# Kernel tuning notes

Measured on AMD Instinct MI355X. Metric: run time of the kernel, lower is better.

The kernel has to match this reference:

```python
import jax, jax.numpy as jnp
import numpy as np

S, D_IN, D_OUT = 4096, 1024, 1024

def setup_inputs() -> dict:
    key = jax.random.key(0)
    kx, kq, kk, kv = jax.random.split(key, 4)
    scale = 0.02
    return {
        "x": jax.random.normal(kx, (S, D_IN), dtype=jnp.float32),
        "W_query": jax.random.normal(kq, (D_IN, D_OUT), dtype=jnp.float32) * scale,
        "W_key": jax.random.normal(kk, (D_IN, D_OUT), dtype=jnp.float32) * scale,
        "W_value": jax.random.normal(kv, (D_IN, D_OUT), dtype=jnp.float32) * scale,
    }

def reference(x, W_query, W_key, W_value):
    # x: [S, d_in]; W_*: [d_in, d_out]
    queries = x @ W_query        # [S, d_out]
    keys = x @ W_key             # [S, d_out]
    values = x @ W_value         # [S, d_out]
    d_k = keys.shape[-1]
    attn_scores = queries @ keys.T            # [S, S]
    attn_weights = jax.nn.softmax(attn_scores / jnp.sqrt(jnp.float32(d_k)), axis=-1)
    context_vec = attn_weights @ values       # [S, d_out]
    return context_vec
```

## Files before the change

### kernel.cpp

```cpp
#include <hip/hip_runtime.h>
#include <hip/hip_bf16.h>

typedef _Float16 f16x8 __attribute__((ext_vector_type(8)));
typedef float f32x4 __attribute__((ext_vector_type(4)));
typedef unsigned short u16;
typedef u16 u16x8 __attribute__((ext_vector_type(8)));
typedef u16 u16x4 __attribute__((ext_vector_type(4)));

__device__ __forceinline__ u16 f2h_bits(float f) {
    _Float16 h = (_Float16)f;
    return __builtin_bit_cast(u16, h);
}
__device__ __forceinline__ float h2f(u16 b) {
    return (float)__builtin_bit_cast(_Float16, b);
}

template <int MODE>
__global__ __launch_bounds__(256, 4) void gemm_bt(
    const u16* __restrict__ A, int lda,
    const u16* __restrict__ B, int ldb,
    u16* __restrict__ C, int ldc,
    int Ksplit, float alpha, size_t c_z_stride,
    int bnW, int bmW, int numPanelX,
    float* __restrict__ rowsum, u16* __restrict__ vt)
{
    __shared__ __attribute__((aligned(16))) u16 As[128 * 32];
    __shared__ __attribute__((aligned(16))) u16 Bs[128 * 32];

    const int t    = threadIdx.x;
    const int lane = t & 63;
    const int wave = t >> 6;
    const int wm   = wave & 1;
    const int wn   = wave >> 1;
    const int l16  = lane & 15;
    const int quad = lane >> 4;

    const int lin = blockIdx.y * gridDim.x + blockIdx.x;
    const int xcd = lin & 7;
    const int idx = lin >> 3;
    const int px  = xcd % numPanelX;
    const int py  = xcd / numPanelX;
    const int bn  = px * bnW + idx % bnW;
    const int bm  = py * bmW + idx / bnW;

    const int kz = blockIdx.z;
    A += (size_t)kz * Ksplit;
    B += (size_t)kz * Ksplit;
    C += (size_t)kz * c_z_stride;

    const int srow = t >> 2;
    const int scol = ((t & 3) ^ ((t >> 3) & 3)) * 8;

    const u16* Ag = A + (size_t)(bm * 128 + srow) * lda + scol;
    const u16* Bg = B + (size_t)(bn * 128 + srow) * ldb + scol;
    const size_t a64 = (size_t)64 * lda;
    const size_t b64 = (size_t)64 * ldb;

    u16* AsD = &As[t * 8];
    u16* BsD = &Bs[t * 8];

    const int fseg = (quad ^ ((l16 >> 1) & 3)) * 8;
    const u16* Afr = &As[(wm * 64 + l16) * 32 + fseg];
    const u16* Bfr = &Bs[(wn * 64 + l16) * 32 + fseg];

    f32x4 acc[4][4] = {};
    float4 pa0, pa1, pb0, pb1;

    pa0 = *(const float4*)(Ag);
    pa1 = *(const float4*)(Ag + a64);
    pb0 = *(const float4*)(Bg);
    pb1 = *(const float4*)(Bg + b64);

    for (int k0 = 0; k0 < Ksplit; k0 += 32) {
        __syncthreads();
        *(float4*)(AsD)        = pa0;
        *(float4*)(AsD + 2048) = pa1;
        *(float4*)(BsD)        = pb0;
        *(float4*)(BsD + 2048) = pb1;
        __syncthreads();

        const int kn = (k0 + 32 < Ksplit) ? k0 + 32 : 0;
        pa0 = *(const float4*)(Ag + kn);
        pa1 = *(const float4*)(Ag + kn + a64);
        pb0 = *(const float4*)(Bg + kn);
        pb1 = *(const float4*)(Bg + kn + b64);

        f16x8 af[4], bfv[4];
#pragma unroll
        for (int i = 0; i < 4; i++) af[i]  = *(const f16x8*)(Afr + i * 512);
#pragma unroll
        for (int i = 0; i < 4; i++) bfv[i] = *(const f16x8*)(Bfr + i * 512);
#pragma unroll
        for (int mi = 0; mi < 4; mi++)
#pragma unroll
            for (int ni = 0; ni < 4; ni++)
                acc[mi][ni] = __builtin_amdgcn_mfma_f32_16x16x32_f16(
                    af[mi], bfv[ni], acc[mi][ni], 0, 0, 0);
    }

    const int crow = bm * 128 + wm * 64 + quad * 4;
    const int ccol = bn * 128 + wn * 64 + l16;

    if (MODE == 1) {
        float rs[4][4];
#pragma unroll
        for (int mi = 0; mi < 4; mi++)
#pragma unroll
            for (int r = 0; r < 4; r++) rs[mi][r] = 0.f;
#pragma unroll
        for (int mi = 0; mi < 4; mi++) {
#pragma unroll
            for (int ni = 0; ni < 4; ni++) {
#pragma unroll
                for (int r = 0; r < 4; r++) {
                    float e = __expf(acc[mi][ni][r] * alpha);
                    rs[mi][r] += e;
                    C[(size_t)(crow + mi * 16 + r) * ldc + (ccol + ni * 16)] = f2h_bits(e);
                }
            }
        }
#pragma unroll
        for (int mi = 0; mi < 4; mi++) {
#pragma unroll
            for (int r = 0; r < 4; r++) {
                float s = rs[mi][r];
#pragma unroll
                for (int o = 1; o < 16; o <<= 1) s += __shfl_xor(s, o);
                if (l16 == 0)
                    atomicAdd(&rowsum[crow + mi * 16 + r], s);
            }
        }
    } else if (MODE == 2 && bn >= 16) {
#pragma unroll
        for (int ni = 0; ni < 4; ni++) {
            const int cV = (bn - 16) * 128 + wn * 64 + ni * 16 + l16;
#pragma unroll
            for (int mi = 0; mi < 4; mi++) {
                u16x4 o;
#pragma unroll
                for (int r = 0; r < 4; r++) o[r] = f2h_bits(acc[mi][ni][r]);
                *(u16x4*)(vt + (size_t)cV * 4096 + crow + mi * 16) = o;
            }
        }
    } else {
#pragma unroll
        for (int mi = 0; mi < 4; mi++)
#pragma unroll
            for (int ni = 0; ni < 4; ni++)
#pragma unroll
                for (int r = 0; r < 4; r++)
                    C[(size_t)(crow + mi * 16 + r) * ldc + (ccol + ni * 16)] =
                        f2h_bits(acc[mi][ni][r] * alpha);
    }
}

__global__ __launch_bounds__(256) void cast_to_f16(
    const float* __restrict__ in, u16* __restrict__ out, int n)
{
    int i = (blockIdx.x * 256 + threadIdx.x) * 4;
    if (i + 3 < n) {
        float4 v = *(const float4*)(in + i);
        ushort4 o;
        o.x = f2h_bits(v.x);
        o.y = f2h_bits(v.y);
        o.z = f2h_bits(v.z);
        o.w = f2h_bits(v.w);
        *(ushort4*)(out + i) = o;
    }
}

__global__ __launch_bounds__(256) void transpose_w3(
    const float* __restrict__ W0, const float* __restrict__ W1,
    const float* __restrict__ W2, u16* __restrict__ out)
{
    const float* in = (blockIdx.z == 0) ? W0 : (blockIdx.z == 1) ? W1 : W2;
    u16* o = out + (size_t)blockIdx.z * 1024 * 1024;
    __shared__ float tile[32][33];
    const int bx = blockIdx.x * 32;
    const int by = blockIdx.y * 32;
    const int tx = threadIdx.x, ty = threadIdx.y;
#pragma unroll
    for (int j = 0; j < 4; j++)
        tile[ty + j * 8][tx] = in[(size_t)(by + ty + j * 8) * 1024 + bx + tx];
    __syncthreads();
#pragma unroll
    for (int j = 0; j < 4; j++)
        o[(size_t)(bx + ty + j * 8) * 1024 + by + tx] = f2h_bits(tile[tx][ty + j * 8]);
}

__global__ __launch_bounds__(256) void zero_f32(float* __restrict__ p, int n)
{
    int i = (blockIdx.x * 256 + threadIdx.x) * 4;
    if (i + 3 < n) *(float4*)(p + i) = float4{0.f, 0.f, 0.f, 0.f};
}

__global__ __launch_bounds__(256) void add_div4(
    const u16* __restrict__ P, const float* __restrict__ l,
    float* __restrict__ o)
{
    const size_t zs = (size_t)4096 * 1024;
    int i = (blockIdx.x * 256 + threadIdx.x) * 8;
    float inv = 1.0f / l[i >> 10];
    float s[8] = {};
#pragma unroll
    for (int z = 0; z < 4; z++) {
        u16x8 h = *(const u16x8*)(P + z * zs + i);
#pragma unroll
        for (int j = 0; j < 8; j++) s[j] += h2f(h[j]);
    }
    float4 lo{s[0] * inv, s[1] * inv, s[2] * inv, s[3] * inv};
    float4 hi{s[4] * inv, s[5] * inv, s[6] * inv, s[7] * inv};
    *(float4*)(o + i) = lo;
    *(float4*)(o + i + 4) = hi;
}

extern "C" void kernel_launch(void* const* d_in, const int* in_sizes, int n_in,
                              void* d_out, int out_size, void* d_ws, size_t ws_size,
                              hipStream_t stream)
{
    (void)in_sizes; (void)n_in; (void)out_size; (void)ws_size;
    const float* x  = (const float*)d_in[0];
    const float* Wq = (const float*)d_in[1];
    const float* Wk = (const float*)d_in[2];
    const float* Wv = (const float*)d_in[3];
    float* out = (float*)d_out;
    char* ws = (char*)d_ws;

    u16* xb  = (u16*)(ws);
    u16* Wt  = (u16*)(ws + ((size_t)8  << 20));
    u16* QK  = (u16*)(ws + ((size_t)14 << 20));
    u16* Sb  = (u16*)(ws + ((size_t)32 << 20));
    u16* Vt  = (u16*)(ws + ((size_t)64 << 20));
    float* lr = (float*)(ws + ((size_t)72 << 20));
    u16* P   = (u16*)(ws);

    const int S = 4096, D = 1024;
    dim3 tb(32, 8);

    cast_to_f16<<<(S * D) / (4 * 256), 256, 0, stream>>>(x, xb, S * D);

    transpose_w3<<<dim3(32, 32, 3), tb, 0, stream>>>(Wq, Wk, Wv, Wt);

    gemm_bt<2><<<dim3(3072 / 128, S / 128, 1), 256, 0, stream>>>(
        xb, D, Wt, D, QK, 2048, D, 1.0f, 0, 6, 16, 4, nullptr, Vt);

    zero_f32<<<S / (4 * 256), 256, 0, stream>>>(lr, S);

    gemm_bt<1><<<dim3(S / 128, S / 128, 1), 256, 0, stream>>>(
        QK, 2048, QK + 1024, 2048, Sb, S, D, 0.03125f, 0, 8, 16, 4, lr, nullptr);

    gemm_bt<0><<<dim3(D / 128, S / 128, 4), 256, 0, stream>>>(
        Sb, S, Vt, S, P, D, 1024, 1.0f, (size_t)S * D, 4, 8, 2, nullptr, nullptr);

    add_div4<<<(S * D) / (8 * 256), 256, 0, stream>>>(P, lr, out);
}
```

Before: 230.2 us.

## Use async global-to-LDS loads with triple-buffered shared memory in GEMM

Replaces the register-staged global loads and LDS stores in the GEMM main loop with direct global_load_lds async copies into a three-stage LDS ring. Each iteration waits on the older loads with waitcnt, issues the load two tiles ahead, and drops one barrier per iteration. This is meant to hide memory latency and cut VGPR staging and LDS store instructions. In exchange LDS use triples and launch bounds drop to 3 blocks per CU. It also relies on the hand-coded waitcnt encoding and on the XOR-swizzled source column matching the per-lane LDS destination layout.

```diff
diff --git a/kernel.cpp b/kernel.cpp
--- a/kernel.cpp
+++ b/kernel.cpp
@@ -15,8 +15,15 @@
     return (float)__builtin_bit_cast(_Float16, b);
 }
 
+__device__ __forceinline__ void async_ld16(const void* g, void* l) {
+    __builtin_amdgcn_global_load_lds(
+        (__attribute__((address_space(1))) void*)(void*)g,
+        (__attribute__((address_space(3))) void*)l,
+        16, 0, 0);
+}
+
 template <int MODE>
-__global__ __launch_bounds__(256, 4) void gemm_bt(
+__global__ __launch_bounds__(256, 3) void gemm_bt(
     const u16* __restrict__ A, int lda,
     const u16* __restrict__ B, int ldb,
     u16* __restrict__ C, int ldc,
@@ -24,8 +31,7 @@
     int bnW, int bmW, int numPanelX,
     float* __restrict__ rowsum, u16* __restrict__ vt)
 {
-    __shared__ __attribute__((aligned(16))) u16 As[128 * 32];
-    __shared__ __attribute__((aligned(16))) u16 Bs[128 * 32];
+    __shared__ __attribute__((aligned(16))) u16 L[3 * 8192];
 
     const int t    = threadIdx.x;
     const int lane = t & 63;
@@ -56,46 +62,48 @@
     const size_t a64 = (size_t)64 * lda;
     const size_t b64 = (size_t)64 * ldb;
 
-    u16* AsD = &As[t * 8];
-    u16* BsD = &Bs[t * 8];
+    u16* l0 = L;
+    u16* l1 = L + 8192;
+    u16* l2 = L + 16384;
 
     const int fseg = (quad ^ ((l16 >> 1) & 3)) * 8;
-    const u16* Afr = &As[(wm * 64 + l16) * 32 + fseg];
-    const u16* Bfr = &Bs[(wn * 64 + l16) * 32 + fseg];
+    const int AfrO = (wm * 64 + l16) * 32 + fseg;
+    const int BfrO = 4096 + (wn * 64 + l16) * 32 + fseg;
 
     f32x4 acc[4][4] = {};
-    float4 pa0, pa1, pb0, pb1;
-
-    pa0 = *(const float4*)(Ag);
-    pa1 = *(const float4*)(Ag + a64);
-    pb0 = *(const float4*)(Bg);
-    pb1 = *(const float4*)(Bg + b64);
-
+
+    auto issue = [&](int koff, u16* buf) {
+        async_ld16(Ag + koff,       buf + t * 8);
+        async_ld16(Ag + koff + a64, buf + 2048 + t * 8);
+        async_ld16(Bg + koff,       buf + 4096 + t * 8);
+        async_ld16(Bg + koff + b64, buf + 6144 + t * 8);
+    };
+
+    issue(0, l0);
+    issue(32, l1);
+
+    u16 *cur = l0, *nxt = l1, *prv = l2;
     for (int k0 = 0; k0 < Ksplit; k0 += 32) {
-        __syncthreads();
-        *(float4*)(AsD)        = pa0;
-        *(float4*)(AsD + 2048) = pa1;
-        *(float4*)(BsD)        = pb0;
-        *(float4*)(BsD + 2048) = pb1;
-        __syncthreads();
-
-        const int kn = (k0 + 32 < Ksplit) ? k0 + 32 : 0;
-        pa0 = *(const float4*)(Ag + kn);
-        pa1 = *(const float4*)(Ag + kn + a64);
-        pb0 = *(const float4*)(Bg + kn);
-        pb1 = *(const float4*)(Bg + kn + b64);
+        __builtin_amdgcn_s_waitcnt(0xF74);
+        __builtin_amdgcn_s_barrier();
+
+        int kf = k0 + 64;
+        if (kf >= Ksplit) kf -= Ksplit;
+        issue(kf, prv);
 
         f16x8 af[4], bfv[4];
 #pragma unroll
-        for (int i = 0; i < 4; i++) af[i]  = *(const f16x8*)(Afr + i * 512);
-#pragma unroll
-        for (int i = 0; i < 4; i++) bfv[i] = *(const f16x8*)(Bfr + i * 512);
+        for (int i = 0; i < 4; i++) af[i]  = *(const f16x8*)(cur + AfrO + i * 512);
+#pragma unroll
+        for (int i = 0; i < 4; i++) bfv[i] = *(const f16x8*)(cur + BfrO + i * 512);
 #pragma unroll
         for (int mi = 0; mi < 4; mi++)
 #pragma unroll
             for (int ni = 0; ni < 4; ni++)
                 acc[mi][ni] = __builtin_amdgcn_mfma_f32_16x16x32_f16(
                     af[mi], bfv[ni], acc[mi][ni], 0, 0, 0);
+
+        u16* tmp = cur; cur = nxt; nxt = prv; prv = tmp;
     }
 
     const int crow = bm * 128 + wm * 64 + quad * 4;
```

After: 229.1 us. No clear change (-0.5%).
